# Kernel optimization log

Measured on AMD Instinct MI355X. Metric: run time of the kernel, lower is better.

The kernel has to match this reference:

```python
import jax, jax.numpy as jnp
import numpy as np

N_NODES = 32768
N_EDGES = 262144
D = 512
NUM_EXPERTS = 4
TOP_K = 2
LAYERS = 2


def setup_inputs() -> dict:
    key = jax.random.key(0)
    ks = jax.random.split(key, 8)
    x = jax.random.normal(ks[0], (N_NODES, D), dtype=jnp.float32)
    edge_index = jax.random.randint(ks[1], (2, N_EDGES), 0, N_NODES, dtype=jnp.int64)
    s = 1.0 / np.sqrt(D)
    # Gating network: Linear(D, num_experts)
    gate_W = jax.random.uniform(ks[2], (D, NUM_EXPERTS), jnp.float32, -s, s)
    gate_b = jax.random.uniform(ks[3], (NUM_EXPERTS,), jnp.float32, -s, s)
    # Per-expert, per-layer SAGEConv params: lin_l (neighbor, with bias) and lin_r (root, no bias)
    Wl = jax.random.uniform(ks[4], (NUM_EXPERTS, LAYERS, D, D), jnp.float32, -s, s)
    bl = jax.random.uniform(ks[5], (NUM_EXPERTS, LAYERS, D), jnp.float32, -s, s)
    Wr = jax.random.uniform(ks[6], (NUM_EXPERTS, LAYERS, D, D), jnp.float32, -s, s)
    return {"x": x, "gate_W": gate_W, "gate_b": gate_b, "Wl": Wl, "bl": bl,
            "Wr": Wr, "edge_index": edge_index}


def reference(x, gate_W, gate_b, Wl, bl, Wr, edge_index):
    n = x.shape[0]
    src, dst = edge_index[0], edge_index[1]

    # Gating: softmax over experts, then top-k (sorted descending, like torch.topk)
    gates = jax.nn.softmax(x @ gate_W + gate_b, axis=-1)          # [N, E]
    top_v, top_i = jax.lax.top_k(gates, TOP_K)                     # [N, K]

    # Mean-aggregation normalization (PyG SAGEConv 'mean': isolated nodes -> 0)
    deg = jax.ops.segment_sum(jnp.ones((src.shape[0],), x.dtype), dst, num_segments=n)
    inv_deg = jnp.where(deg > 0, 1.0 / jnp.maximum(deg, 1.0), 0.0)[:, None]  # [N,1]

    def sage_conv(h, W_l, b_l, W_r):
        # mean of neighbor messages, then lin_l(aggr) + lin_r(h)
        aggr = jax.ops.segment_sum(h[src], dst, num_segments=n) * inv_deg
        return aggr @ W_l + b_l + h @ W_r

    # Dense all-expert forward (module runs every expert), small fixed loop over experts
    expert_outs = []
    for e in range(NUM_EXPERTS):
        h = x
        for l in range(LAYERS):
            h = sage_conv(h, Wl[e, l], bl[e, l], Wr[e, l])
            h = jax.nn.relu(h)  # norm='id', dropout=0 (eval), last_activation=True
        expert_outs.append(h)
    expert_outputs = jnp.stack(expert_outs, axis=1)                # [N, E, D]

    # Gather top-k expert outputs and combine with gate weights
    sel = jnp.take_along_axis(expert_outputs, top_i[:, :, None], axis=1)  # [N, K, D]
    out = jnp.sum(sel * top_v[:, :, None], axis=1)                 # [N, D]
    return out
```

## Files before the change

### kernel.cpp

```cpp
#include <hip/hip_runtime.h>

typedef unsigned short u16;
typedef unsigned int u32;
typedef u16 u16x8 __attribute__((ext_vector_type(8)));
typedef short s16x8 __attribute__((ext_vector_type(8)));
typedef float f32x4 __attribute__((ext_vector_type(4)));

#define NN 32768
#define EE 262144
#define DD 512
#define WMAT (512 * 1024)

__device__ __forceinline__ float b2f(u16 u) {
    return __uint_as_float(((u32)u) << 16);
}
__device__ __forceinline__ u16 f2b(float f) {
    u32 u = __float_as_uint(f);
    u32 r = (u + 0x7FFFu + ((u >> 16) & 1u)) >> 16;
    return (u16)r;
}

__global__ void detect_kernel(const u32* __restrict__ ei, int* __restrict__ flags) {
    if (threadIdx.x == 0) {
        int allzero = 1;
        for (int i = 0; i < 64; ++i)
            if (ei[2 * i + 1] != 0u) allzero = 0;
        flags[0] = allzero;
    }
}

__global__ void edges_kernel(const u32* __restrict__ ei, const int* __restrict__ flags,
                             int* __restrict__ s32, int* __restrict__ d32) {
    int t = blockIdx.x * 256 + threadIdx.x;
    u32 s, d;
    if (flags[0]) {
        s = ei[2 * t];
        d = ei[2 * EE + 2 * t];
    } else {
        s = ei[t];
        d = ei[EE + t];
    }
    s32[t] = (int)(s & (NN - 1));
    d32[t] = (int)(d & (NN - 1));
}

__global__ void transpose_kernel(const float* __restrict__ Wl, const float* __restrict__ Wr,
                                 u16* __restrict__ Bt) {
    int bid = blockIdx.x;
    int matid = bid >> 8;
    int tile = bid & 255;
    int em = matid >> 1;
    int half = matid & 1;
    const float* W = (half ? Wr : Wl) + (size_t)em * DD * DD;
    u16* out = Bt + (size_t)em * DD * 1024 + half * DD;
    int tk = (tile >> 4) * 32, tn = (tile & 15) * 32;
    __shared__ float s[32][33];
    int t = threadIdx.x;
    int rr = t >> 5, cc = t & 31;
#pragma unroll
    for (int p = 0; p < 4; ++p) {
        int kr = p * 8 + rr;
        s[kr][cc] = W[(size_t)(tk + kr) * DD + tn + cc];
    }
    __syncthreads();
#pragma unroll
    for (int p = 0; p < 4; ++p) {
        int nr = p * 8 + rr;
        out[(size_t)(tn + nr) * 1024 + tk + cc] = f2b(s[cc][nr]);
    }
}

__global__ void gate_kernel(const float* __restrict__ x, const float* __restrict__ gw,
                            const float* __restrict__ gb, float* __restrict__ wg) {
    int node = blockIdx.x * 4 + (threadIdx.x >> 6);
    int l = threadIdx.x & 63;
    const f32x4* xr = (const f32x4*)(x + (size_t)node * DD) + l * 2;
    f32x4 x0 = xr[0], x1 = xr[1];
    float a0 = 0.f, a1 = 0.f, a2 = 0.f, a3 = 0.f;
#pragma unroll
    for (int j = 0; j < 8; ++j) {
        float xf = (j < 4) ? x0[j & 3] : x1[j & 3];
        f32x4 wr = ((const f32x4*)gw)[l * 8 + j];
        a0 += xf * wr[0]; a1 += xf * wr[1]; a2 += xf * wr[2]; a3 += xf * wr[3];
    }
#pragma unroll
    for (int off = 32; off > 0; off >>= 1) {
        a0 += __shfl_down(a0, off, 64);
        a1 += __shfl_down(a1, off, 64);
        a2 += __shfl_down(a2, off, 64);
        a3 += __shfl_down(a3, off, 64);
    }
    if (l == 0) {
        float lg[4] = {a0 + gb[0], a1 + gb[1], a2 + gb[2], a3 + gb[3]};
        float m = fmaxf(fmaxf(lg[0], lg[1]), fmaxf(lg[2], lg[3]));
        float p[4]; float s = 0.f;
#pragma unroll
        for (int e = 0; e < 4; ++e) { p[e] = expf(lg[e] - m); s += p[e]; }
        float inv = 1.f / s;
#pragma unroll
        for (int e = 0; e < 4; ++e) p[e] *= inv;
        int i0 = 0;
#pragma unroll
        for (int e = 1; e < 4; ++e) if (p[e] > p[i0]) i0 = e;
        int i1 = -1;
#pragma unroll
        for (int e = 0; e < 4; ++e) if (e != i0 && (i1 < 0 || p[e] > p[i1])) i1 = e;
        float o[4] = {0.f, 0.f, 0.f, 0.f};
        o[i0] = p[i0]; o[i1] = p[i1];
        float* w = wg + (size_t)node * 4;
        w[0] = o[0]; w[1] = o[1]; w[2] = o[2]; w[3] = o[3];
    }
}

__global__ void gateconv_kernel(const float* __restrict__ x, const float* __restrict__ gw,
                                const float* __restrict__ gb, float* __restrict__ wg,
                                u16* __restrict__ xb) {
    int node = blockIdx.x * 4 + (threadIdx.x >> 6);
    int l = threadIdx.x & 63;
    const f32x4* xr = (const f32x4*)(x + (size_t)node * DD) + l * 2;
    f32x4 x0 = xr[0], x1 = xr[1];
    u16x8 o8;
    o8[0] = f2b(x0[0]); o8[1] = f2b(x0[1]); o8[2] = f2b(x0[2]); o8[3] = f2b(x0[3]);
    o8[4] = f2b(x1[0]); o8[5] = f2b(x1[1]); o8[6] = f2b(x1[2]); o8[7] = f2b(x1[3]);
    *((u16x8*)(xb + (size_t)node * DD) + l) = o8;
    float a0 = 0.f, a1 = 0.f, a2 = 0.f, a3 = 0.f;
#pragma unroll
    for (int j = 0; j < 8; ++j) {
        float xf = (j < 4) ? x0[j & 3] : x1[j & 3];
        f32x4 wr = ((const f32x4*)gw)[l * 8 + j];
        a0 += xf * wr[0]; a1 += xf * wr[1]; a2 += xf * wr[2]; a3 += xf * wr[3];
    }
#pragma unroll
    for (int off = 32; off > 0; off >>= 1) {
        a0 += __shfl_down(a0, off, 64);
        a1 += __shfl_down(a1, off, 64);
        a2 += __shfl_down(a2, off, 64);
        a3 += __shfl_down(a3, off, 64);
    }
    if (l == 0) {
        float lg[4] = {a0 + gb[0], a1 + gb[1], a2 + gb[2], a3 + gb[3]};
        float m = fmaxf(fmaxf(lg[0], lg[1]), fmaxf(lg[2], lg[3]));
        float p[4]; float s = 0.f;
#pragma unroll
        for (int e = 0; e < 4; ++e) { p[e] = expf(lg[e] - m); s += p[e]; }
        float inv = 1.f / s;
#pragma unroll
        for (int e = 0; e < 4; ++e) p[e] *= inv;
        int i0 = 0;
#pragma unroll
        for (int e = 1; e < 4; ++e) if (p[e] > p[i0]) i0 = e;
        int i1 = -1;
#pragma unroll
        for (int e = 0; e < 4; ++e) if (e != i0 && (i1 < 0 || p[e] > p[i1])) i1 = e;
        float o[4] = {0.f, 0.f, 0.f, 0.f};
        o[i0] = p[i0]; o[i1] = p[i1];
        float* w = wg + (size_t)node * 4;
        w[0] = o[0]; w[1] = o[1]; w[2] = o[2]; w[3] = o[3];
    }
}

__global__ void compact_kernel(const float* __restrict__ wg, int* __restrict__ cnt,
                               int* __restrict__ list, int* __restrict__ posn) {
    int node = blockIdx.x * 256 + threadIdx.x;
    const float* w = wg + (size_t)node * 4;
#pragma unroll
    for (int e = 0; e < 4; ++e)
        if (w[e] > 0.f) {
            int p = atomicAdd(&cnt[e], 1);
            list[e * NN + p] = node;
            posn[node * 4 + e] = p;
        }
}

__global__ void tilemap_kernel(int* __restrict__ cnt, int* __restrict__ tmap) {
    if (threadIdx.x == 0) {
        int T = 0, acc = 0;
        for (int e = 0; e < 4; ++e) {
            cnt[4 + e] = acc;
            int c = cnt[e];
            acc += c;
            int nt = (c + 127) >> 7;
            for (int i = 0; i < nt; ++i) tmap[T++] = (e << 16) | i;
        }
        cnt[8] = T;
    }
}

__global__ void deg_kernel(const int* __restrict__ dst, int* __restrict__ deg) {
    int t = blockIdx.x * blockDim.x + threadIdx.x;
    if (t < EE) atomicAdd(&deg[dst[t]], 1);
}

__global__ void scan1_kernel(const int* __restrict__ deg, int* __restrict__ start,
                             float* __restrict__ invd, int* __restrict__ bsum) {
    int t = threadIdx.x;
    int idx = blockIdx.x * 1024 + t;
    int v = deg[idx];
    int sc = v;
#pragma unroll
    for (int off = 1; off < 64; off <<= 1) {
        int u = __shfl_up(sc, off, 64);
        if ((t & 63) >= off) sc += u;
    }
    __shared__ int wsum[16], woff[16];
    if ((t & 63) == 63) wsum[t >> 6] = sc;
    __syncthreads();
    if (t == 0) {
        int acc = 0;
        for (int w = 0; w < 16; ++w) { woff[w] = acc; acc += wsum[w]; }
        bsum[blockIdx.x] = acc;
    }
    __syncthreads();
    start[idx] = woff[t >> 6] + sc - v;
    invd[idx] = v > 0 ? 1.0f / (float)v : 0.0f;
}

__global__ void scan2_kernel(int* __restrict__ bsum, int* __restrict__ boff) {
    if (threadIdx.x == 0) {
        int acc = 0;
        for (int b = 0; b < 32; ++b) { boff[b] = acc; acc += bsum[b]; }
    }
}

__global__ void scan3_kernel(int* __restrict__ start, int* __restrict__ cursor,
                             const int* __restrict__ boff) {
    int idx = blockIdx.x * 256 + threadIdx.x;
    int s = start[idx] + boff[idx >> 10];
    start[idx] = s;
    cursor[idx] = s;
}

__global__ void scatter_kernel(const int* __restrict__ src, const int* __restrict__ dst,
                               int* __restrict__ cursor, int* __restrict__ csr) {
    int t = blockIdx.x * blockDim.x + threadIdx.x;
    if (t < EE) {
        int d = dst[t];
        int pos = atomicAdd(&cursor[d], 1);
        csr[pos] = src[t];
    }
}

template <bool F32IN>
__global__ void aggr_kernel(const void* __restrict__ hv, u16* __restrict__ outB,
                            const int* __restrict__ start, const int* __restrict__ deg,
                            const int* __restrict__ csr, const float* __restrict__ invd,
                            const float* __restrict__ wg, int eBase, size_t stride) {
    int eo = blockIdx.x >> 13;
    int node = ((blockIdx.x & 8191) << 2) + (threadIdx.x >> 6);
    int expert = eBase + eo;
    if (wg != nullptr && wg[(size_t)node * 4 + expert] == 0.f) return;
    int l = threadIdx.x & 63;
    int s0 = start[node];
    int dg = deg[node];
    u16* out = outB + (size_t)eo * stride;
    const u16* hB = (const u16*)hv + (size_t)eo * stride;
    const float* hF = (const float*)hv + (size_t)eo * stride;
    float a[8] = {0.f, 0.f, 0.f, 0.f, 0.f, 0.f, 0.f, 0.f};

    for (int base = 0; base < dg; base += 64) {
        int cnt = dg - base;
        if (cnt > 64) cnt = 64;
        int vidx = 0;
        if (l < cnt) vidx = csr[s0 + base + l];
        int q = 0;
        if (!F32IN) {
            for (; q + 8 <= cnt; q += 8) {
                int j0 = __shfl(vidx, q, 64);
                int j1 = __shfl(vidx, q + 1, 64);
                int j2 = __shfl(vidx, q + 2, 64);
                int j3 = __shfl(vidx, q + 3, 64);
                int j4 = __shfl(vidx, q + 4, 64);
                int j5 = __shfl(vidx, q + 5, 64);
                int j6 = __shfl(vidx, q + 6, 64);
                int j7 = __shfl(vidx, q + 7, 64);
                u16x8 v0 = *((const u16x8*)(hB + (size_t)j0 * DD) + l);
                u16x8 v1 = *((const u16x8*)(hB + (size_t)j1 * DD) + l);
                u16x8 v2 = *((const u16x8*)(hB + (size_t)j2 * DD) + l);
                u16x8 v3 = *((const u16x8*)(hB + (size_t)j3 * DD) + l);
                u16x8 v4 = *((const u16x8*)(hB + (size_t)j4 * DD) + l);
                u16x8 v5 = *((const u16x8*)(hB + (size_t)j5 * DD) + l);
                u16x8 v6 = *((const u16x8*)(hB + (size_t)j6 * DD) + l);
                u16x8 v7 = *((const u16x8*)(hB + (size_t)j7 * DD) + l);
#pragma unroll
                for (int q2 = 0; q2 < 8; ++q2)
                    a[q2] += ((b2f(v0[q2]) + b2f(v1[q2])) + (b2f(v2[q2]) + b2f(v3[q2]))) +
                             ((b2f(v4[q2]) + b2f(v5[q2])) + (b2f(v6[q2]) + b2f(v7[q2])));
            }
        }
        for (; q + 4 <= cnt; q += 4) {
            int j0 = __shfl(vidx, q, 64);
            int j1 = __shfl(vidx, q + 1, 64);
            int j2 = __shfl(vidx, q + 2, 64);
            int j3 = __shfl(vidx, q + 3, 64);
            if (F32IN) {
                const f32x4* r0 = (const f32x4*)(hF + (size_t)j0 * DD) + l * 2;
                const f32x4* r1 = (const f32x4*)(hF + (size_t)j1 * DD) + l * 2;
                const f32x4* r2 = (const f32x4*)(hF + (size_t)j2 * DD) + l * 2;
                const f32x4* r3 = (const f32x4*)(hF + (size_t)j3 * DD) + l * 2;
                f32x4 u0 = r0[0], u1 = r0[1];
                f32x4 u2 = r1[0], u3 = r1[1];
                f32x4 u4 = r2[0], u5 = r2[1];
                f32x4 u6 = r3[0], u7 = r3[1];
#pragma unroll
                for (int q2 = 0; q2 < 4; ++q2) {
                    a[q2] += (u0[q2] + u2[q2]) + (u4[q2] + u6[q2]);
                    a[4 + q2] += (u1[q2] + u3[q2]) + (u5[q2] + u7[q2]);
                }
            } else {
                u16x8 v0 = *((const u16x8*)(hB + (size_t)j0 * DD) + l);
                u16x8 v1 = *((const u16x8*)(hB + (size_t)j1 * DD) + l);
                u16x8 v2 = *((const u16x8*)(hB + (size_t)j2 * DD) + l);
                u16x8 v3 = *((const u16x8*)(hB + (size_t)j3 * DD) + l);
#pragma unroll
                for (int q2 = 0; q2 < 8; ++q2)
                    a[q2] += (b2f(v0[q2]) + b2f(v1[q2])) + (b2f(v2[q2]) + b2f(v3[q2]));
            }
        }
        for (; q < cnt; ++q) {
            int j = __shfl(vidx, q, 64);
            if (F32IN) {
                const f32x4* r = (const f32x4*)(hF + (size_t)j * DD) + l * 2;
                f32x4 u0 = r[0], u1 = r[1];
#pragma unroll
                for (int q2 = 0; q2 < 4; ++q2) { a[q2] += u0[q2]; a[4 + q2] += u1[q2]; }
            } else {
                u16x8 v = *((const u16x8*)(hB + (size_t)j * DD) + l);
#pragma unroll
                for (int q2 = 0; q2 < 8; ++q2) a[q2] += b2f(v[q2]);
            }
        }
    }
    float sc = invd[node];
    u16x8 o;
#pragma unroll
    for (int q2 = 0; q2 < 8; ++q2) o[q2] = f2b(a[q2] * sc);
    *((u16x8*)(out + (size_t)node * DD) + l) = o;
}

__global__ void aggr2_kernel(const u16* __restrict__ h, u16* __restrict__ outC,
                             const int* __restrict__ start, const int* __restrict__ deg,
                             const int* __restrict__ csr, const float* __restrict__ invd,
                             const float* __restrict__ wg, const int* __restrict__ posn,
                             const int* __restrict__ cntb) {
    const int node = (blockIdx.x << 2) + (threadIdx.x >> 6);
    const int l = threadIdx.x & 63;
    const float* w = wg + (size_t)node * 4;
    int e0 = -1, e1 = -1;
#pragma unroll
    for (int e = 0; e < 4; ++e) {
        if (w[e] > 0.f) { if (e0 < 0) e0 = e; else e1 = e; }
    }
    if (e0 < 0) return;
    const int dual = (e1 >= 0);
    if (!dual) e1 = e0;
    const size_t STRE = (size_t)NN * DD;
    const u16* hA = h + (size_t)e0 * STRE;
    const u16* hC = h + (size_t)e1 * STRE;
    const int g0 = cntb[4 + e0] + posn[node * 4 + e0];
    const int g1 = cntb[4 + e1] + posn[node * 4 + e1];
    const int s0 = start[node];
    const int dg = deg[node];
    float a0[8] = {0.f, 0.f, 0.f, 0.f, 0.f, 0.f, 0.f, 0.f};
    float a1[8] = {0.f, 0.f, 0.f, 0.f, 0.f, 0.f, 0.f, 0.f};

    for (int base = 0; base < dg; base += 64) {
        int cnt = dg - base;
        if (cnt > 64) cnt = 64;
        int vidx = 0;
        if (l < cnt) vidx = csr[s0 + base + l];
        int q = 0;
        for (; q + 4 <= cnt; q += 4) {
            int j0 = __shfl(vidx, q, 64);
            int j1 = __shfl(vidx, q + 1, 64);
            int j2 = __shfl(vidx, q + 2, 64);
            int j3 = __shfl(vidx, q + 3, 64);
            u16x8 u0 = *((const u16x8*)(hA + (size_t)j0 * DD) + l);
            u16x8 u1 = *((const u16x8*)(hA + (size_t)j1 * DD) + l);
            u16x8 u2 = *((const u16x8*)(hA + (size_t)j2 * DD) + l);
            u16x8 u3 = *((const u16x8*)(hA + (size_t)j3 * DD) + l);
            u16x8 t0 = *((const u16x8*)(hC + (size_t)j0 * DD) + l);
            u16x8 t1 = *((const u16x8*)(hC + (size_t)j1 * DD) + l);
            u16x8 t2 = *((const u16x8*)(hC + (size_t)j2 * DD) + l);
            u16x8 t3 = *((const u16x8*)(hC + (size_t)j3 * DD) + l);
#pragma unroll
            for (int q2 = 0; q2 < 8; ++q2) {
                a0[q2] += (b2f(u0[q2]) + b2f(u1[q2])) + (b2f(u2[q2]) + b2f(u3[q2]));
                a1[q2] += (b2f(t0[q2]) + b2f(t1[q2])) + (b2f(t2[q2]) + b2f(t3[q2]));
            }
        }
        for (; q < cnt; ++q) {
            int j = __shfl(vidx, q, 64);
            u16x8 u = *((const u16x8*)(hA + (size_t)j * DD) + l);
            u16x8 t = *((const u16x8*)(hC + (size_t)j * DD) + l);
#pragma unroll
            for (int q2 = 0; q2 < 8; ++q2) { a0[q2] += b2f(u[q2]); a1[q2] += b2f(t[q2]); }
        }
    }
    float sc = invd[node];
    u16x8 o0, o1;
#pragma unroll
    for (int q2 = 0; q2 < 8; ++q2) { o0[q2] = f2b(a0[q2] * sc); o1[q2] = f2b(a1[q2] * sc); }
    *((u16x8*)(outC + (size_t)g0 * DD) + l) = o0;
    if (dual)
        *((u16x8*)(outC + (size_t)g1 * DD) + l) = o1;
}

__device__ __forceinline__ void gload16(const void* g, void* l) {
    __builtin_amdgcn_global_load_lds((const __attribute__((address_space(1))) void*)g,
                                     (__attribute__((address_space(3))) void*)l, 16, 0, 0);
}

template <bool A2F32>
__global__ void __launch_bounds__(256, 4) gemm_kernel(
    const u16* __restrict__ A1, const u16* __restrict__ A2b, const float* __restrict__ A2f,
    size_t sA, const u16* __restrict__ Bt, size_t sBt,
    const float* __restrict__ bias, size_t sBias,
    u16* __restrict__ Hout, size_t sH, float* __restrict__ Out,
    const float* __restrict__ wg, int mode, int eBase, int ntt) {
    __shared__ u16 lds[A2F32 ? 12288 : 8192];
    u16* ldsA = lds;
    float* ldsF = (float*)lds;
    u16* ldsB = lds + (A2F32 ? 8192 : 4096);
    const int tid = threadIdx.x;
    const int lane = tid & 63;
    const int w = tid >> 6;

    const int bid = blockIdx.x;
    const int xcd = bid & 7;
    const int local = bid >> 3;
    const int mtl = local / ntt;
    const int sub = local - mtl * ntt;
    const int expert = sub >> 2;
    const int wgE = eBase + expert;
    const int m0 = (xcd * 32 + mtl) * 128;
    const int n0 = (sub & 3) * 128;

    const u16* A1p = A1 + (size_t)expert * sA;
    const u16* A2p = A2b + (size_t)expert * sA;
    const u16* Btp = Bt + (size_t)expert * sBt;
    const float* biasp = bias + (size_t)expert * sBias;
    u16* Houtp = Hout + (size_t)expert * sH;

    const int wm = (w >> 1) * 64;
    const int wn = (w & 1) * 64;

    f32x4 acc[4][4];
#pragma unroll
    for (int i = 0; i < 4; ++i)
#pragma unroll
        for (int j = 0; j < 4; ++j) acc[i][j] = (f32x4){0.f, 0.f, 0.f, 0.f};

    const int p0 = tid, p1 = 256 + tid;
    const int r0 = p0 >> 2, c0 = ((p0 & 3) - (r0 >> 1)) & 3;
    const int r1 = p1 >> 2, c1 = ((p1 & 3) - (r1 >> 1)) & 3;
    const int arow = lane & 15;
    const int kc = lane >> 4;

    for (int kb = 0; kb < 32; ++kb) {
        __syncthreads();
        if (!A2F32 || kb < 16) {
            const u16* As = (kb < 16) ? A1p : A2p;
            const int kcol = (kb & 15) * 32;
            gload16(As + (size_t)(m0 + r0) * DD + kcol + c0 * 8, ldsA + p0 * 8);
            gload16(As + (size_t)(m0 + r1) * DD + kcol + c1 * 8, ldsA + p1 * 8);
        } else {
            const float* Af = A2f + (size_t)m0 * DD + (kb - 16) * 32;
#pragma unroll
            for (int q = 0; q < 4; ++q) {
                int p = q * 256 + tid;
                int rr = p >> 3, cpos = p & 7, cc2 = (cpos - rr) & 7;
                gload16(Af + (size_t)rr * DD + cc2 * 4, ldsF + p * 4);
            }
        }
        gload16(Btp + (size_t)(n0 + r0) * 1024 + kb * 32 + c0 * 8, ldsB + p0 * 8);
        gload16(Btp + (size_t)(n0 + r1) * 1024 + kb * 32 + c1 * 8, ldsB + p1 * 8);
        __syncthreads();
        s16x8 af[4], bf[4];
        if (!A2F32 || kb < 16) {
#pragma unroll
            for (int f = 0; f < 4; ++f) {
                int ra = wm + f * 16 + arow;
                int pa = (kc + (ra >> 1)) & 3;
                af[f] = *(const s16x8*)(ldsA + (ra * 4 + pa) * 8);
            }
        } else {
#pragma unroll
            for (int f = 0; f < 4; ++f) {
                int ra = wm + f * 16 + arow;
                int plo = ra * 8 + ((2 * kc + ra) & 7);
                int phi = ra * 8 + ((2 * kc + 1 + ra) & 7);
                f32x4 lo = *(const f32x4*)(ldsF + plo * 4);
                f32x4 hi = *(const f32x4*)(ldsF + phi * 4);
                s16x8 t;
                t[0] = (short)f2b(lo[0]); t[1] = (short)f2b(lo[1]);
                t[2] = (short)f2b(lo[2]); t[3] = (short)f2b(lo[3]);
                t[4] = (short)f2b(hi[0]); t[5] = (short)f2b(hi[1]);
                t[6] = (short)f2b(hi[2]); t[7] = (short)f2b(hi[3]);
                af[f] = t;
            }
        }
#pragma unroll
        for (int f = 0; f < 4; ++f) {
            int rb = wn + f * 16 + arow;
            int pb = (kc + (rb >> 1)) & 3;
            bf[f] = *(const s16x8*)(ldsB + (rb * 4 + pb) * 8);
        }
#pragma unroll
        for (int i = 0; i < 4; ++i)
#pragma unroll
            for (int j = 0; j < 4; ++j)
                acc[i][j] = __builtin_amdgcn_mfma_f32_16x16x32_bf16(af[i], bf[j], acc[i][j], 0, 0, 0);
    }

    const int colq = lane & 15;
    const int rq = lane >> 4;
#pragma unroll
    for (int i = 0; i < 4; ++i) {
#pragma unroll
        for (int j = 0; j < 4; ++j) {
            int col = n0 + wn + j * 16 + colq;
            float bv = biasp[col];
#pragma unroll
            for (int r = 0; r < 4; ++r) {
                int row = m0 + wm + i * 16 + rq * 4 + r;
                float v = fmaxf(acc[i][j][r] + bv, 0.f);
                size_t idx = (size_t)row * DD + col;
                if (mode == 0) {
                    Houtp[idx] = f2b(v);
                } else {
                    float wv = wg[(size_t)row * 4 + wgE];
                    if (mode == 1) {
                        Out[idx] = wv * v;
                    } else if (mode == 2) {
                        if (wv > 0.f) Out[idx] += wv * v;
                    } else {
                        if (wv > 0.f) unsafeAtomicAdd(&Out[idx], wv * v);
                    }
                }
            }
        }
    }
}

__global__ void __launch_bounds__(256, 4) gemm_gather_kernel(
    const u16* __restrict__ A1c, const u16* __restrict__ A2,
    const u16* __restrict__ Bt, const float* __restrict__ bias,
    float* __restrict__ Out, const float* __restrict__ wg,
    const int* __restrict__ list, const int* __restrict__ cntb,
    const int* __restrict__ tmap) {
    const int xcd = blockIdx.x & 7;
    const int local = blockIdx.x >> 3;
    const int j4 = local & 3;
    const int slot = local >> 2;
    const int t = slot * 8 + xcd;
    if (t >= cntb[8]) return;
    const u32 mi = (u32)tmap[t];
    const int e = mi >> 16;
    const int mt = mi & 0xffff;
    const int cntE = cntb[e];
    const int eb = cntb[4 + e];
    const int base = mt << 7;
    const int n0 = j4 * 128;

    __shared__ u16 lds[8192];
    u16* ldsA = lds;
    u16* ldsB = lds + 4096;
    const int tid = threadIdx.x;
    const int lane = tid & 63;
    const int w = tid >> 6;

    const size_t STRE = (size_t)NN * DD;
    const u16* A2p = A2 + (size_t)e * STRE;
    const u16* Btp = Bt + (size_t)e * (2 * WMAT);
    const float* biasp = bias + (size_t)e * 1024;
    const int* listE = list + e * NN;

    const int wm = (w >> 1) * 64;
    const int wn = (w & 1) * 64;

    f32x4 acc[4][4];
#pragma unroll
    for (int i = 0; i < 4; ++i)
#pragma unroll
        for (int j = 0; j < 4; ++j) acc[i][j] = (f32x4){0.f, 0.f, 0.f, 0.f};

    const int p0 = tid, p1 = 256 + tid;
    const int r0 = p0 >> 2, c0 = ((p0 & 3) - (r0 >> 1)) & 3;
    const int r1 = p1 >> 2, c1 = ((p1 & 3) - (r1 >> 1)) & 3;
    int g0 = eb + base + r0; if (g0 > 2 * NN - 1) g0 = 2 * NN - 1;
    int g1 = eb + base + r1; if (g1 > 2 * NN - 1) g1 = 2 * NN - 1;
    int q0 = base + r0; if (q0 >= cntE) q0 = cntE - 1;
    int q1 = base + r1; if (q1 >= cntE) q1 = cntE - 1;
    const int gr0 = listE[q0];
    const int gr1 = listE[q1];
    const int arow = lane & 15;
    const int kc = lane >> 4;

    for (int kb = 0; kb < 32; ++kb) {
        __syncthreads();
        if (kb < 16) {
            const int kcol = kb * 32;
            gload16(A1c + (size_t)g0 * DD + kcol + c0 * 8, ldsA + p0 * 8);
            gload16(A1c + (size_t)g1 * DD + kcol + c1 * 8, ldsA + p1 * 8);
        } else {
            const int kcol = (kb - 16) * 32;
            gload16(A2p + (size_t)gr0 * DD + kcol + c0 * 8, ldsA + p0 * 8);
            gload16(A2p + (size_t)gr1 * DD + kcol + c1 * 8, ldsA + p1 * 8);
        }
        gload16(Btp + (size_t)(n0 + r0) * 1024 + kb * 32 + c0 * 8, ldsB + p0 * 8);
        gload16(Btp + (size_t)(n0 + r1) * 1024 + kb * 32 + c1 * 8, ldsB + p1 * 8);
        __syncthreads();
        s16x8 af[4], bf[4];
#pragma unroll
        for (int f = 0; f < 4; ++f) {
            int ra = wm + f * 16 + arow;
            int pa = (kc + (ra >> 1)) & 3;
            af[f] = *(const s16x8*)(ldsA + (ra * 4 + pa) * 8);
        }
#pragma unroll
        for (int f = 0; f < 4; ++f) {
            int rb = wn + f * 16 + arow;
            int pb = (kc + (rb >> 1)) & 3;
            bf[f] = *(const s16x8*)(ldsB + (rb * 4 + pb) * 8);
        }
#pragma unroll
        for (int i = 0; i < 4; ++i)
#pragma unroll
            for (int j = 0; j < 4; ++j)
                acc[i][j] = __builtin_amdgcn_mfma_f32_16x16x32_bf16(af[i], bf[j], acc[i][j], 0, 0, 0);
    }

    const int colq = lane & 15;
    const int rq = lane >> 4;
#pragma unroll
    for (int i = 0; i < 4; ++i) {
        int nd[4]; float wv4[4]; bool val[4];
#pragma unroll
        for (int r = 0; r < 4; ++r) {
            int rowl = base + wm + i * 16 + rq * 4 + r;
            val[r] = rowl < cntE;
            int qq = val[r] ? rowl : 0;
            nd[r] = listE[qq];
            wv4[r] = wg[(size_t)nd[r] * 4 + e];
        }
#pragma unroll
        for (int j = 0; j < 4; ++j) {
            int col = n0 + wn + j * 16 + colq;
            float bv = biasp[col];
#pragma unroll
            for (int r = 0; r < 4; ++r) {
                if (val[r]) {
                    float v = fmaxf(acc[i][j][r] + bv, 0.f);
                    unsafeAtomicAdd(&Out[(size_t)nd[r] * DD + col], wv4[r] * v);
                }
            }
        }
    }
}

extern "C" void kernel_launch(void* const* d_in, const int* in_sizes, int n_in,
                              void* d_out, int out_size, void* d_ws, size_t ws_size,
                              hipStream_t stream) {
    const float* x  = (const float*)d_in[0];
    const float* gW = (const float*)d_in[1];
    const float* gb = (const float*)d_in[2];
    const float* Wl = (const float*)d_in[3];
    const float* bl = (const float*)d_in[4];
    const float* Wr = (const float*)d_in[5];
    const u32*   ei = (const u32*)d_in[6];
    float* outp = (float*)d_out;

    char* ws = (char*)d_ws;
    size_t off = 0;
    auto alloc = [&](size_t bytes) -> void* {
        void* p = ws + off;
        off += (bytes + 255) & ~(size_t)255;
        return p;
    };
    const size_t MB32 = (size_t)NN * DD * 2;
    const size_t STR = (size_t)NN * DD;
    int*   flags  = (int*)alloc(512);
    float* wg     = (float*)alloc((size_t)NN * 4 * 4);
    int*   deg    = (int*)alloc((size_t)NN * 4);
    int*   start  = (int*)alloc((size_t)NN * 4);
    int*   cursor = (int*)alloc((size_t)NN * 4);
    float* invd   = (float*)alloc((size_t)NN * 4);
    int*   src32  = (int*)alloc((size_t)EE * 4);
    int*   dst32  = (int*)alloc((size_t)EE * 4);
    int*   csr    = (int*)alloc((size_t)EE * 4);
    u16*   Bt     = (u16*)alloc((size_t)8 * WMAT * 2);
    int*   cnt    = (int*)alloc(64);
    int*   tmap   = (int*)alloc(1040 * 4);
    int*   list   = dst32;
    int*   posn   = src32;

    size_t rem = (ws_size > off) ? ws_size - off : 0;
    int tier;
    if      (rem >= 7 * MB32 + 65536) tier = 0;
    else if (rem >= 6 * MB32 + 65536) tier = 2;
    else if (rem >= 5 * MB32 + 65536) tier = 3;
    else if (rem >= 4 * MB32 + 65536) tier = 4;
    else                              tier = 5;

    u16 *xb = nullptr, *h1 = nullptr, *aggr1 = nullptr, *aggr0 = nullptr;
    if (tier == 0) {
        xb = (u16*)alloc(MB32);
        h1 = (u16*)alloc(4 * MB32);
        aggr1 = (u16*)alloc(2 * MB32);
        aggr0 = aggr1;
    } else if (tier == 2) {
        xb = (u16*)alloc(MB32);
        h1 = (u16*)alloc(4 * MB32);
        aggr1 = (u16*)alloc(MB32);
        aggr0 = aggr1;
    } else if (tier == 3) {
        aggr0 = (u16*)alloc(MB32);
        h1 = (u16*)alloc(4 * MB32);
        aggr1 = aggr0;
    } else if (tier == 4) {
        aggr0 = (u16*)alloc(MB32);
        xb = (u16*)alloc(MB32);
        h1 = (u16*)alloc(MB32);
        aggr1 = (u16*)alloc(MB32);
    } else {
        aggr0 = (u16*)alloc(MB32);
        h1 = (u16*)alloc(MB32);
        aggr1 = (u16*)alloc(MB32);
    }

    int* bsum = flags + 16;
    int* boff = flags + 64;

    hipMemsetAsync(deg, 0, (size_t)NN * 4, stream);

    detect_kernel<<<1, 64, 0, stream>>>(ei, flags);
    edges_kernel<<<EE / 256, 256, 0, stream>>>(ei, flags, src32, dst32);
    transpose_kernel<<<16 * 256, 256, 0, stream>>>(Wl, Wr, Bt);
    if (xb != nullptr)
        gateconv_kernel<<<NN / 4, 256, 0, stream>>>(x, gW, gb, wg, xb);
    else
        gate_kernel<<<NN / 4, 256, 0, stream>>>(x, gW, gb, wg);
    deg_kernel<<<EE / 256, 256, 0, stream>>>(dst32, deg);
    scan1_kernel<<<32, 1024, 0, stream>>>(deg, start, invd, bsum);
    scan2_kernel<<<1, 64, 0, stream>>>(bsum, boff);
    scan3_kernel<<<NN / 256, 256, 0, stream>>>(start, cursor, boff);
    scatter_kernel<<<EE / 256, 256, 0, stream>>>(src32, dst32, cursor, csr);

    if (tier == 0) {
        hipMemsetAsync(cnt, 0, 64, stream);
        compact_kernel<<<NN / 256, 256, 0, stream>>>(wg, cnt, list, posn);
        tilemap_kernel<<<1, 64, 0, stream>>>(cnt, tmap);
        aggr_kernel<false><<<8192, 256, 0, stream>>>(xb, aggr0, start, deg, csr, invd,
                                                     nullptr, 0, 0);
        gemm_kernel<false><<<256 * 16, 256, 0, stream>>>(
            aggr0, xb, nullptr, 0, Bt, 2 * WMAT, bl, 1024,
            h1, STR, nullptr, wg, 0, 0, 16);
        hipMemsetAsync(outp, 0, (size_t)NN * DD * 4, stream);
        aggr2_kernel<<<8192, 256, 0, stream>>>(h1, aggr1, start, deg, csr, invd, wg,
                                               posn, cnt);
        gemm_gather_kernel<<<65 * 4 * 8, 256, 0, stream>>>(
            aggr1, h1, Bt + WMAT, bl + 512, outp, wg, list, cnt, tmap);
    } else if (tier == 2) {
        aggr_kernel<false><<<8192, 256, 0, stream>>>(xb, aggr0, start, deg, csr, invd,
                                                     nullptr, 0, 0);
        gemm_kernel<false><<<256 * 16, 256, 0, stream>>>(
            aggr0, xb, nullptr, 0, Bt, 2 * WMAT, bl, 1024,
            h1, STR, nullptr, wg, 0, 0, 16);
        for (int e = 0; e < 4; ++e) {
            aggr_kernel<false><<<8192, 256, 0, stream>>>(
                h1 + (size_t)e * STR, aggr1, start, deg, csr, invd, wg, e, 0);
            gemm_kernel<false><<<256 * 4, 256, 0, stream>>>(
                aggr1, h1 + (size_t)e * STR, nullptr, 0,
                Bt + (size_t)(e * 2 + 1) * WMAT, 0, bl + (e * 2 + 1) * 512, 0,
                nullptr, 0, outp, wg, (e == 0) ? 1 : 2, e, 4);
        }
    } else if (tier == 3) {
        aggr_kernel<true><<<8192, 256, 0, stream>>>(x, aggr0, start, deg, csr, invd,
                                                    nullptr, 0, 0);
        gemm_kernel<true><<<256 * 16, 256, 0, stream>>>(
            aggr0, nullptr, x, 0, Bt, 2 * WMAT, bl, 1024,
            h1, STR, nullptr, wg, 0, 0, 16);
        for (int e = 0; e < 4; ++e) {
            aggr_kernel<false><<<8192, 256, 0, stream>>>(
                h1 + (size_t)e * STR, aggr1, start, deg, csr, invd, wg, e, 0);
            gemm_kernel<false><<<256 * 4, 256, 0, stream>>>(
                aggr1, h1 + (size_t)e * STR, nullptr, 0,
                Bt + (size_t)(e * 2 + 1) * WMAT, 0, bl + (e * 2 + 1) * 512, 0,
                nullptr, 0, outp, wg, (e == 0) ? 1 : 2, e, 4);
        }
    } else {
        if (tier == 4) {
            aggr_kernel<false><<<8192, 256, 0, stream>>>(xb, aggr0, start, deg, csr, invd,
                                                         nullptr, 0, 0);
        } else {
            aggr_kernel<true><<<8192, 256, 0, stream>>>(x, aggr0, start, deg, csr, invd,
                                                        nullptr, 0, 0);
        }
        for (int e = 0; e < 4; ++e) {
            const u16* BtL0 = Bt + (size_t)(e * 2 + 0) * WMAT;
            const u16* BtL1 = Bt + (size_t)(e * 2 + 1) * WMAT;
            const float* b0 = bl + (e * 2 + 0) * 512;
            const float* b1 = bl + (e * 2 + 1) * 512;
            if (tier == 4)
                gemm_kernel<false><<<256 * 4, 256, 0, stream>>>(
                    aggr0, xb, nullptr, 0, BtL0, 0, b0, 0, h1, 0, nullptr, wg, 0, e, 4);
            else
                gemm_kernel<true><<<256 * 4, 256, 0, stream>>>(
                    aggr0, nullptr, x, 0, BtL0, 0, b0, 0, h1, 0, nullptr, wg, 0, e, 4);
            aggr_kernel<false><<<8192, 256, 0, stream>>>(h1, aggr1, start, deg, csr, invd,
                                                         wg, e, 0);
            gemm_kernel<false><<<256 * 4, 256, 0, stream>>>(
                aggr1, h1, nullptr, 0, BtL1, 0, b1, 0, nullptr, 0, outp, wg,
                (e == 0) ? 1 : 2, e, 4);
        }
    }
}
```

Baseline: 725.5 us.

## Split gated gather GEMM into primary/secondary passes to drop atomics and memset

Nodes are compacted into separate primary-expert and secondary-expert lists, and the final gather GEMM runs as two launches. The first writes the output directly and the second accumulates with plain read-modify-write, which removes the output memset and the float atomics. The GEMM tile also shrinks from 128x128 to 128x64 with higher launch bounds, which should raise occupancy. In exchange there is an extra launch, the A tile is reloaded for each N slice, and correctness depends on each node appearing at most once per pass.

```diff
diff --git a/kernel.cpp b/kernel.cpp
--- a/kernel.cpp
+++ b/kernel.cpp
@@ -160,29 +160,46 @@
 }
 
 __global__ void compact_kernel(const float* __restrict__ wg, int* __restrict__ cnt,
-                               int* __restrict__ list, int* __restrict__ posn) {
+                               int* __restrict__ lists, int* __restrict__ posn) {
     int node = blockIdx.x * 256 + threadIdx.x;
     const float* w = wg + (size_t)node * 4;
+    int e0 = -1, e1 = -1;
 #pragma unroll
     for (int e = 0; e < 4; ++e)
-        if (w[e] > 0.f) {
-            int p = atomicAdd(&cnt[e], 1);
-            list[e * NN + p] = node;
-            posn[node * 4 + e] = p;
-        }
-}
-
-__global__ void tilemap_kernel(int* __restrict__ cnt, int* __restrict__ tmap) {
+        if (w[e] > 0.f) { if (e0 < 0) e0 = e; else e1 = e; }
+    if (e0 >= 0) {
+        int p = atomicAdd(&cnt[e0], 1);
+        lists[e0 * NN + p] = node;
+        posn[node * 2] = p;
+    }
+    if (e1 >= 0) {
+        int p = atomicAdd(&cnt[4 + e1], 1);
+        lists[(4 + e1) * NN + p] = node;
+        posn[node * 2 + 1] = p;
+    }
+}
+
+__global__ void tilemap_kernel(int* __restrict__ cnt, int* __restrict__ tmapP,
+                               int* __restrict__ tmapS) {
     if (threadIdx.x == 0) {
         int T = 0, acc = 0;
         for (int e = 0; e < 4; ++e) {
-            cnt[4 + e] = acc;
+            cnt[8 + e] = acc;
             int c = cnt[e];
             acc += c;
             int nt = (c + 127) >> 7;
-            for (int i = 0; i < nt; ++i) tmap[T++] = (e << 16) | i;
-        }
-        cnt[8] = T;
+            for (int i = 0; i < nt; ++i) tmapP[T++] = (e << 16) | i;
+        }
+        cnt[16] = T;
+        T = 0; acc = 0;
+        for (int e = 0; e < 4; ++e) {
+            cnt[12 + e] = acc;
+            int c = cnt[4 + e];
+            acc += c;
+            int nt = (c + 127) >> 7;
+            for (int i = 0; i < nt; ++i) tmapS[T++] = (e << 16) | i;
+        }
+        cnt[17] = T;
     }
 }
 
@@ -356,8 +373,8 @@
     const size_t STRE = (size_t)NN * DD;
     const u16* hA = h + (size_t)e0 * STRE;
     const u16* hC = h + (size_t)e1 * STRE;
-    const int g0 = cntb[4 + e0] + posn[node * 4 + e0];
-    const int g1 = cntb[4 + e1] + posn[node * 4 + e1];
+    const int g0 = cntb[8 + e0] + posn[node * 2];
+    const int g1 = NN + cntb[12 + e1] + posn[node * 2 + 1];
     const int s0 = start[node];
     const int dg = deg[node];
     float a0[8] = {0.f, 0.f, 0.f, 0.f, 0.f, 0.f, 0.f, 0.f};
@@ -542,27 +559,28 @@
     }
 }
 
-__global__ void __launch_bounds__(256, 4) gemm_gather_kernel(
+template <int SEC>
+__global__ void __launch_bounds__(256, 5) gemm_gather_kernel(
     const u16* __restrict__ A1c, const u16* __restrict__ A2,
     const u16* __restrict__ Bt, const float* __restrict__ bias,
     float* __restrict__ Out, const float* __restrict__ wg,
-    const int* __restrict__ list, const int* __restrict__ cntb,
+    const int* __restrict__ lists, const int* __restrict__ cntb,
     const int* __restrict__ tmap) {
     const int xcd = blockIdx.x & 7;
     const int local = blockIdx.x >> 3;
-    const int j4 = local & 3;
-    const int slot = local >> 2;
+    const int j8 = local & 7;
+    const int slot = local >> 3;
     const int t = slot * 8 + xcd;
-    if (t >= cntb[8]) return;
+    if (t >= cntb[16 + SEC]) return;
     const u32 mi = (u32)tmap[t];
     const int e = mi >> 16;
     const int mt = mi & 0xffff;
-    const int cntE = cntb[e];
-    const int eb = cntb[4 + e];
+    const int cntE = cntb[SEC * 4 + e];
+    const int eb = (SEC ? NN : 0) + cntb[8 + SEC * 4 + e];
     const int base = mt << 7;
-    const int n0 = j4 * 128;
-
-    __shared__ u16 lds[8192];
+    const int n0 = j8 * 64;
+
+    __shared__ u16 lds[6144];
     u16* ldsA = lds;
     u16* ldsB = lds + 4096;
     const int tid = threadIdx.x;
@@ -573,14 +591,13 @@
     const u16* A2p = A2 + (size_t)e * STRE;
     const u16* Btp = Bt + (size_t)e * (2 * WMAT);
     const float* biasp = bias + (size_t)e * 1024;
-    const int* listE = list + e * NN;
-
-    const int wm = (w >> 1) * 64;
-    const int wn = (w & 1) * 64;
-
-    f32x4 acc[4][4];
-#pragma unroll
-    for (int i = 0; i < 4; ++i)
+    const int* listE = lists + (SEC * 4 + e) * NN;
+
+    const int wm = w * 32;
+
+    f32x4 acc[2][4];
+#pragma unroll
+    for (int i = 0; i < 2; ++i)
 #pragma unroll
         for (int j = 0; j < 4; ++j) acc[i][j] = (f32x4){0.f, 0.f, 0.f, 0.f};
 
@@ -608,23 +625,22 @@
             gload16(A2p + (size_t)gr1 * DD + kcol + c1 * 8, ldsA + p1 * 8);
         }
         gload16(Btp + (size_t)(n0 + r0) * 1024 + kb * 32 + c0 * 8, ldsB + p0 * 8);
-        gload16(Btp + (size_t)(n0 + r1) * 1024 + kb * 32 + c1 * 8, ldsB + p1 * 8);
         __syncthreads();
-        s16x8 af[4], bf[4];
-#pragma unroll
-        for (int f = 0; f < 4; ++f) {
+        s16x8 af[2], bf[4];
+#pragma unroll
+        for (int f = 0; f < 2; ++f) {
             int ra = wm + f * 16 + arow;
             int pa = (kc + (ra >> 1)) & 3;
             af[f] = *(const s16x8*)(ldsA + (ra * 4 + pa) * 8);
         }
 #pragma unroll
-        for (int f = 0; f < 4; ++f) {
-            int rb = wn + f * 16 + arow;
+        for (int g = 0; g < 4; ++g) {
+            int rb = g * 16 + arow;
             int pb = (kc + (rb >> 1)) & 3;
-            bf[f] = *(const s16x8*)(ldsB + (rb * 4 + pb) * 8);
-        }
-#pragma unroll
-        for (int i = 0; i < 4; ++i)
+            bf[g] = *(const s16x8*)(ldsB + (rb * 4 + pb) * 8);
+        }
+#pragma unroll
+        for (int i = 0; i < 2; ++i)
 #pragma unroll
             for (int j = 0; j < 4; ++j)
                 acc[i][j] = __builtin_amdgcn_mfma_f32_16x16x32_bf16(af[i], bf[j], acc[i][j], 0, 0, 0);
@@ -633,25 +649,27 @@
     const int colq = lane & 15;
     const int rq = lane >> 4;
 #pragma unroll
-    for (int i = 0; i < 4; ++i) {
+    for (int f = 0; f < 2; ++f) {
         int nd[4]; float wv4[4]; bool val[4];
 #pragma unroll
         for (int r = 0; r < 4; ++r) {
-            int rowl = base + wm + i * 16 + rq * 4 + r;
+            int rowl = base + wm + f * 16 + rq * 4 + r;
             val[r] = rowl < cntE;
             int qq = val[r] ? rowl : 0;
             nd[r] = listE[qq];
             wv4[r] = wg[(size_t)nd[r] * 4 + e];
         }
 #pragma unroll
-        for (int j = 0; j < 4; ++j) {
-            int col = n0 + wn + j * 16 + colq;
+        for (int g = 0; g < 4; ++g) {
+            int col = n0 + g * 16 + colq;
             float bv = biasp[col];
 #pragma unroll
             for (int r = 0; r < 4; ++r) {
                 if (val[r]) {
-                    float v = fmaxf(acc[i][j][r] + bv, 0.f);
-                    unsafeAtomicAdd(&Out[(size_t)nd[r] * DD + col], wv4[r] * v);
+                    float v = fmaxf(acc[f][g][r] + bv, 0.f);
+                    size_t idx = (size_t)nd[r] * DD + col;
+                    if (SEC) Out[idx] += wv4[r] * v;
+                    else     Out[idx] = wv4[r] * v;
                 }
             }
         }
@@ -689,9 +707,9 @@
     int*   dst32  = (int*)alloc((size_t)EE * 4);
     int*   csr    = (int*)alloc((size_t)EE * 4);
     u16*   Bt     = (u16*)alloc((size_t)8 * WMAT * 2);
-    int*   cnt    = (int*)alloc(64);
+    int*   cnt    = (int*)alloc(128);
     int*   tmap   = (int*)alloc(1040 * 4);
-    int*   list   = dst32;
+    int*   lists  = dst32;
     int*   posn   = src32;
 
     size_t rem = (ws_size > off) ? ws_size - off : 0;
@@ -747,19 +765,20 @@
     scatter_kernel<<<EE / 256, 256, 0, stream>>>(src32, dst32, cursor, csr);
 
     if (tier == 0) {
-        hipMemsetAsync(cnt, 0, 64, stream);
-        compact_kernel<<<NN / 256, 256, 0, stream>>>(wg, cnt, list, posn);
-        tilemap_kernel<<<1, 64, 0, stream>>>(cnt, tmap);
+        hipMemsetAsync(cnt, 0, 32, stream);
+        compact_kernel<<<NN / 256, 256, 0, stream>>>(wg, cnt, lists, posn);
+        tilemap_kernel<<<1, 64, 0, stream>>>(cnt, tmap, tmap + 520);
         aggr_kernel<false><<<8192, 256, 0, stream>>>(xb, aggr0, start, deg, csr, invd,
                                                      nullptr, 0, 0);
         gemm_kernel<false><<<256 * 16, 256, 0, stream>>>(
             aggr0, xb, nullptr, 0, Bt, 2 * WMAT, bl, 1024,
             h1, STR, nullptr, wg, 0, 0, 16);
-        hipMemsetAsync(outp, 0, (size_t)NN * DD * 4, stream);
         aggr2_kernel<<<8192, 256, 0, stream>>>(h1, aggr1, start, deg, csr, invd, wg,
                                                posn, cnt);
-        gemm_gather_kernel<<<65 * 4 * 8, 256, 0, stream>>>(
-            aggr1, h1, Bt + WMAT, bl + 512, outp, wg, list, cnt, tmap);
+        gemm_gather_kernel<0><<<33 * 8 * 8, 256, 0, stream>>>(
+            aggr1, h1, Bt + WMAT, bl + 512, outp, wg, lists, cnt, tmap);
+        gemm_gather_kernel<1><<<33 * 8 * 8, 256, 0, stream>>>(
+            aggr1, h1, Bt + WMAT, bl + 512, outp, wg, lists, cnt, tmap + 520);
     } else if (tier == 2) {
         aggr_kernel<false><<<8192, 256, 0, stream>>>(xb, aggr0, start, deg, csr, invd,
                                                      nullptr, 0, 0);
```

Result: slower. 1.101 ms (+51.8%).
